# Kernel optimization log

Measured on AMD Instinct MI355X. Metric: run time of the kernel, lower is better.

## Reference

```python
import math
import jax, jax.numpy as jnp
from jax import lax
import numpy as np

LN_EPS = 1e-5
K = 3          # deform-conv kernel size
PAD = 1        # 'same' padding so offset map matches output resolution


def setup_inputs() -> dict:
    key = jax.random.key(0)
    ks = jax.random.split(key, 6)
    B, C, H, W, Co = 4, 256, 64, 64, 256
    x = jax.random.normal(ks[0], (B, C, H, W), jnp.float32)
    dwc_w = jax.random.normal(ks[1], (C, 1, K, K), jnp.float32) * 0.02
    ln_w = jnp.ones((C,), jnp.float32)
    ln_b = jnp.zeros((C,), jnp.float32)
    fcd_w = jax.random.normal(ks[2], (1, C, 1, 1), jnp.float32) * 0.02
    fca_w = jax.random.normal(ks[3], (1, C, 1, 1), jnp.float32) * 0.02
    fan_in = C * K * K
    dconv_w = jax.random.normal(ks[4], (Co, C, K, K), jnp.float32) / math.sqrt(fan_in)
    dconv_b = jnp.zeros((Co,), jnp.float32)
    return dict(x=x, dwc_w=dwc_w, ln_w=ln_w, ln_b=ln_b,
                fcd_w=fcd_w, fca_w=fca_w, dconv_w=dconv_w, dconv_b=dconv_b)


def _bilinear_sample(x, py, px):
    # x: [B,C,H,W]; py/px: [B,KK,H,W] float sample positions (zero-padded border)
    B, C, H, W = x.shape
    y0 = jnp.floor(py); x0 = jnp.floor(px)
    y1 = y0 + 1.0;      x1 = x0 + 1.0
    wy1 = py - y0; wy0 = 1.0 - wy1
    wx1 = px - x0; wx0 = 1.0 - wx1

    def gather(yy, xx):
        valid = ((yy >= 0) & (yy < H) & (xx >= 0) & (xx < W)).astype(x.dtype)
        iy = jnp.clip(yy, 0, H - 1).astype(jnp.int32)
        ix = jnp.clip(xx, 0, W - 1).astype(jnp.int32)
        # per-batch fancy gather -> [B,C,KK,H,W]
        v = jax.vmap(lambda img, a, b: img[:, a, b])(x, iy, ix)
        return v * valid[:, None]

    return (gather(y0, x0) * (wy0 * wx0)[:, None]
          + gather(y0, x1) * (wy0 * wx1)[:, None]
          + gather(y1, x0) * (wy1 * wx0)[:, None]
          + gather(y1, x1) * (wy1 * wx1)[:, None])


def reference(x, dwc_w, ln_w, ln_b, fcd_w, fca_w, dconv_w, dconv_b):
    B, C, H, W = x.shape
    KK = K * K
    # --- offset branch ---
    h = lax.conv_general_dilated(x, dwc_w, (1, 1), ((1, 1), (1, 1)),
                                 dimension_numbers=('NCHW', 'OIHW', 'NCHW'),
                                 feature_group_count=C)
    mu = h.mean(axis=1, keepdims=True)
    var = h.var(axis=1, keepdims=True)
    h = (h - mu) * lax.rsqrt(var + LN_EPS)
    h = h * ln_w[None, :, None, None] + ln_b[None, :, None, None]
    h = jax.nn.relu(h)
    r = jax.nn.relu(jnp.einsum('bchw,oc->bohw', h, fcd_w[:, :, 0, 0]))      # [B,1,H,W]
    t = jnp.einsum('bchw,oc->bohw', h, fca_w[:, :, 0, 0])
    theta = (t / (1.0 + jnp.abs(t))) * (math.pi / 180.0)                     # softsign * pi/180
    ox = r * jnp.cos(theta)
    oy = r * jnp.sin(theta)
    # torch code: offsets = cat([ox tiled KK, oy tiled KK], dim=1) -> [B,2KK,H,W]
    off = jnp.concatenate([jnp.tile(ox, (1, KK, 1, 1)), jnp.tile(oy, (1, KK, 1, 1))], axis=1)
    # torchvision DeformConv2d convention: channel 2k = dy, channel 2k+1 = dx
    dy = off[:, 0::2]   # [B,KK,H,W]
    dx = off[:, 1::2]
    # --- deformable sampling ---
    ky = jnp.repeat(jnp.arange(K), K).astype(x.dtype)   # kernel row per tap
    kx = jnp.tile(jnp.arange(K), K).astype(x.dtype)     # kernel col per tap
    py = (jnp.arange(H, dtype=x.dtype) - PAD)[None, None, :, None] + ky[None, :, None, None] + dy
    px = (jnp.arange(W, dtype=x.dtype) - PAD)[None, None, None, :] + kx[None, :, None, None] + dx
    sampled = _bilinear_sample(x, py, px)               # [B,C,KK,H,W]
    Co = dconv_w.shape[0]
    out = jnp.einsum('bckhw,ock->bohw', sampled, dconv_w.reshape(Co, C, KK))
    return out + dconv_b[None, :, None, None]
```

## Files before the change

kernel.cpp:

```cpp
#include <hip/hip_runtime.h>
#include <hip/hip_bf16.h>

#define B_   4
#define C_   256
#define CO_  256
#define H_   64
#define W_   64
#define HW_  4096

typedef __attribute__((ext_vector_type(8))) short short8;
typedef __attribute__((ext_vector_type(4))) float f32x4;
typedef __attribute__((ext_vector_type(2))) float f32x2;

static __device__ __forceinline__ unsigned short f2bf(float f) {
    unsigned u = __builtin_bit_cast(unsigned, f);
    unsigned r = (u + 0x7fffu + ((u >> 16) & 1u)) >> 16;
    return (unsigned short)r;
}
static __device__ __forceinline__ f32x2 pk_mul(f32x2 a, f32x2 b) {
    f32x2 d; asm("v_pk_mul_f32 %0, %1, %2" : "=v"(d) : "v"(a), "v"(b)); return d;
}
static __device__ __forceinline__ f32x2 pk_fma(f32x2 a, f32x2 b, f32x2 c) {
    f32x2 d; asm("v_pk_fma_f32 %0, %1, %2, %3" : "=v"(d) : "v"(a), "v"(b), "v"(c)); return d;
}
static __device__ __forceinline__ f32x2 pk_add(f32x2 a, f32x2 b) {
    f32x2 d; asm("v_pk_add_f32 %0, %1, %2" : "=v"(d) : "v"(a), "v"(b)); return d;
}
static __device__ __forceinline__ unsigned cvtpk(float a, float b) {
    unsigned r; asm("v_cvt_pk_bf16_f32 %0, %1, %2" : "=v"(r) : "v"(a), "v"(b)); return r;
}
static __device__ __forceinline__ f32x2 unpack_bf2(unsigned d) {
    f32x2 v;
    v.x = __builtin_bit_cast(float, d << 16);
    v.y = __builtin_bit_cast(float, d & 0xffff0000u);
    return v;
}

__global__ void k_transpose(const float* __restrict__ x, unsigned short* __restrict__ xT)
{
    __shared__ float t[32][132];
    int bid = blockIdx.x;
    int b   = bid >> 8;
    int rem = bid & 255;
    int hwT = rem >> 1, cT = rem & 1;
    int hw0 = hwT * 32, c0 = cT * 128;
    int tid = threadIdx.x;
    const float* src = x + (size_t)b * C_ * HW_;
    {
        int hw4 = (tid & 7) << 2;
        int cr  = tid >> 3;
#pragma unroll
        for (int it = 0; it < 4; ++it) {
            int c = cr + it * 32;
            f32x4 v = *(const f32x4*)(src + (size_t)(c0 + c) * HW_ + hw0 + hw4);
            t[hw4 + 0][c] = v.x;
            t[hw4 + 1][c] = v.y;
            t[hw4 + 2][c] = v.z;
            t[hw4 + 3][c] = v.w;
        }
    }
    __syncthreads();
    {
        int c8  = (tid & 15) << 3;
        int hwr = tid >> 4;
        unsigned short* dst = xT + (size_t)(((b << 12) + hw0) * 256) + c0 + c8;
#pragma unroll
        for (int it = 0; it < 2; ++it) {
            int hw = hwr + it * 16;
            f32x4 va = *(const f32x4*)&t[hw][c8];
            f32x4 vb = *(const f32x4*)&t[hw][c8 + 4];
            uint4 u;
            u.x = cvtpk(va.x, va.y);
            u.y = cvtpk(va.z, va.w);
            u.z = cvtpk(vb.x, vb.y);
            u.w = cvtpk(vb.z, vb.w);
            *(uint4*)(dst + (size_t)hw * 256) = u;
        }
    }
}

__global__ void k_packB(const float* __restrict__ w, unsigned short* __restrict__ Bt,
                        const float* __restrict__ dwc_w, float* __restrict__ dwcT)
{
    int bid = blockIdx.x;
    int tid = threadIdx.x;
    if (bid < 9) dwcT[bid * 256 + tid] = dwc_w[tid * 9 + bid];
    int e = bid * 256 + tid;
    int j   = e & 7;
    int l4  = (e >> 3) & 3;
    int l15 = (e >> 5) & 15;
    int ks  = (e >> 9) & 7;
    int og  = (e >> 12) & 15;
    int k   = e >> 16;
    int o = og * 16 + l15;
    int c = ks * 32 + l4 * 8 + j;
    Bt[e] = f2bf(w[(o * C_ + c) * 9 + k]);
}

__launch_bounds__(512, 4)
__global__ void k_main(const unsigned short* __restrict__ xT,
                       const float* __restrict__ dwcT,
                       const float* __restrict__ ln_w,
                       const float* __restrict__ ln_b,
                       const float* __restrict__ fcd_w,
                       const float* __restrict__ fca_w,
                       const unsigned short* __restrict__ Bt,
                       const float* __restrict__ bias,
                       float* __restrict__ out)
{
    __shared__ __align__(16) unsigned char smem[33024];

    int tid = threadIdx.x;
    int bi = blockIdx.x;
    int g = ((bi & 7) << 6) | (bi >> 3);
    int p0 = g << 5;
    int b = p0 >> 12;
    int y = (p0 >> 6) & 63;
    int xh = p0 & 63;

    int lane = tid & 63, wid = tid >> 6;
    int l15 = lane & 15, l4 = lane >> 4;

    int gpos = tid >> 4;
    int csub = tid & 15;
    const unsigned short* xb = xT + (size_t)b * HW_ * C_;
    const char* xbB = (const char*)xb;

    float ox, oy;
    {
        int ch0 = csub << 4;
        f32x2 acc2[8];
#pragma unroll
        for (int i = 0; i < 8; ++i) { acc2[i].x = 0.f; acc2[i].y = 0.f; }
#pragma unroll
        for (int j = 0; j < 9; ++j) {
            int gy = y + j / 3 - 1, gx = xh + gpos + j % 3 - 1;
            if (gy >= 0 && gy < H_ && gx >= 0 && gx < W_) {
                const unsigned short* p = xb + (size_t)((gy << 6) + gx) * 256 + ch0;
                short8 rlo = *(const short8*)(p);
                short8 rhi = *(const short8*)(p + 8);
                const float* wrow = dwcT + j * 256 + ch0;
#pragma unroll
                for (int q = 0; q < 4; ++q) {
                    f32x4 wv = *(const f32x4*)(wrow + q * 4);
                    f32x2 w01v; w01v.x = wv.x; w01v.y = wv.y;
                    f32x2 w23v; w23v.x = wv.z; w23v.y = wv.w;
                    unsigned lo = (q < 2) ? ((unsigned*)&rlo)[q * 2] : ((unsigned*)&rhi)[(q - 2) * 2];
                    unsigned hi = (q < 2) ? ((unsigned*)&rlo)[q * 2 + 1] : ((unsigned*)&rhi)[(q - 2) * 2 + 1];
                    acc2[q * 2 + 0] = pk_fma(unpack_bf2(lo), w01v, acc2[q * 2 + 0]);
                    acc2[q * 2 + 1] = pk_fma(unpack_bf2(hi), w23v, acc2[q * 2 + 1]);
                }
            }
        }
        f32x2 sum2, sq2;
        sum2.x = 0.f; sum2.y = 0.f; sq2.x = 0.f; sq2.y = 0.f;
#pragma unroll
        for (int i = 0; i < 8; ++i) {
            sum2 = pk_add(sum2, acc2[i]);
            sq2  = pk_fma(acc2[i], acc2[i], sq2);
        }
        float s1 = sum2.x + sum2.y, s2 = sq2.x + sq2.y;
#pragma unroll
        for (int m = 1; m <= 8; m <<= 1) {
            s1 += __shfl_xor(s1, m);
            s2 += __shfl_xor(s2, m);
        }
        float mu  = s1 * (1.f / 256.f);
        float var = s2 * (1.f / 256.f) - mu * mu;
        float rs  = rsqrtf(var + 1e-5f);
        float d1 = 0.f, d2 = 0.f;
#pragma unroll
        for (int q = 0; q < 4; ++q) {
            f32x4 lwv = *(const f32x4*)(ln_w  + ch0 + q * 4);
            f32x4 lbv = *(const f32x4*)(ln_b  + ch0 + q * 4);
            f32x4 fdv = *(const f32x4*)(fcd_w + ch0 + q * 4);
            f32x4 fav = *(const f32x4*)(fca_w + ch0 + q * 4);
#pragma unroll
            for (int i = 0; i < 4; ++i) {
                float av = (i & 1) ? acc2[q * 2 + (i >> 1)].y : acc2[q * 2 + (i >> 1)].x;
                float hn = (av - mu) * rs * lwv[i] + lbv[i];
                hn = fmaxf(hn, 0.f);
                d1 = fmaf(hn, fdv[i], d1);
                d2 = fmaf(hn, fav[i], d2);
            }
        }
#pragma unroll
        for (int m = 1; m <= 8; m <<= 1) {
            d1 += __shfl_xor(d1, m);
            d2 += __shfl_xor(d2, m);
        }
        float r0 = fmaxf(d1, 0.f);
        float theta = d2 / (1.f + fabsf(d2)) * 0.017453292519943295f;
        ox = r0 * cosf(theta);
        oy = r0 * sinf(theta);
    }

    f32x4 acc[2][2];
#pragma unroll
    for (int m = 0; m < 2; ++m)
#pragma unroll
        for (int n = 0; n < 2; ++n) {
            acc[m][n].x = 0.f; acc[m][n].y = 0.f; acc[m][n].z = 0.f; acc[m][n].w = 0.f;
        }

    const unsigned short* bwave = Bt + (unsigned)(wid * 2) * 4096u
                                     + (unsigned)(l15 * 32 + l4 * 8);
    unsigned rowb = (unsigned)gpos * 512u;
    unsigned csub16 = (unsigned)csub << 4;
    unsigned swzcol = csub16 ^ (((unsigned)gpos & 7u) << 4);

#define GADDR(k)                                                                  \
        int ky = (k) / 3, kx = (k) - ky * 3;                                      \
        float dyv = ((k) <= 4) ? ox : oy;                                         \
        float dxv = ((k) <= 3) ? ox : oy;                                         \
        float py = (float)(y - 1 + ky) + dyv;                                     \
        float px = (float)(xh + gpos - 1 + kx) + dxv;                             \
        float y0f = floorf(py), x0f = floorf(px);                                 \
        int y0 = (int)y0f, x0 = (int)x0f;                                         \
        int y1 = y0 + 1, x1 = x0 + 1;                                             \
        float wy1 = py - y0f, wy0 = 1.f - wy1;                                    \
        float wx1 = px - x0f, wx0 = 1.f - wx1;                                    \
        float vy0 = (y0 >= 0 && y0 < H_) ? 1.f : 0.f;                             \
        float vy1 = (y1 >= 0 && y1 < H_) ? 1.f : 0.f;                             \
        float vx0 = (x0 >= 0 && x0 < W_) ? 1.f : 0.f;                             \
        float vx1 = (x1 >= 0 && x1 < W_) ? 1.f : 0.f;                             \
        w00 = wy0 * wx0 * vy0 * vx0; w01 = wy0 * wx1 * vy0 * vx1;                 \
        w10 = wy1 * wx0 * vy1 * vx0; w11 = wy1 * wx1 * vy1 * vx1;                 \
        int y0c = min(max(y0, 0), H_ - 1), y1c = min(max(y1, 0), H_ - 1);         \
        int x0c = min(max(x0, 0), W_ - 1), x1c = min(max(x1, 0), W_ - 1);         \
        o00 = (unsigned)((y0c << 6) + x0c) * 512u + csub16;                       \
        o01 = (unsigned)((y0c << 6) + x1c) * 512u + csub16;                       \
        o10 = (unsigned)((y1c << 6) + x0c) * 512u + csub16;                       \
        o11 = (unsigned)((y1c << 6) + x1c) * 512u + csub16;

#define GATHER_TAP(k, buf)                                                        \
    {   unsigned o00, o01, o10, o11;                                              \
        float w00, w01, w10, w11;                                                 \
        GADDR(k);                                                                 \
        f32x2 W00, W01, W10, W11;                                                 \
        W00.x = w00; W00.y = w00; W01.x = w01; W01.y = w01;                       \
        W10.x = w10; W10.y = w10; W11.x = w11; W11.y = w11;                       \
        unsigned wb = (unsigned)(buf) * 16384u + rowb + swzcol;                   \
        _Pragma("unroll")                                                         \
        for (int cq = 0; cq < 2; ++cq) {                                          \
            short8 r00 = *(const short8*)(xbB + o00 + cq * 256);                  \
            short8 r01 = *(const short8*)(xbB + o01 + cq * 256);                  \
            short8 r10 = *(const short8*)(xbB + o10 + cq * 256);                  \
            short8 r11 = *(const short8*)(xbB + o11 + cq * 256);                  \
            uint4 pkv;                                                            \
            _Pragma("unroll")                                                     \
            for (int dw = 0; dw < 4; ++dw) {                                      \
                f32x2 a2 = pk_mul(unpack_bf2(((unsigned*)&r00)[dw]), W00);        \
                a2 = pk_fma(unpack_bf2(((unsigned*)&r01)[dw]), W01, a2);          \
                a2 = pk_fma(unpack_bf2(((unsigned*)&r10)[dw]), W10, a2);          \
                a2 = pk_fma(unpack_bf2(((unsigned*)&r11)[dw]), W11, a2);          \
                ((unsigned*)&pkv)[dw] = cvtpk(a2.x, a2.y);                        \
            }                                                                     \
            *(uint4*)(smem + wb + cq * 256) = pkv;                                \
        }                                                                         \
    }

    GATHER_TAP(0, 0);
    __syncthreads();

#pragma unroll
    for (int k = 0; k < 9; ++k) {
        int t = k & 1;
        {
            const unsigned short* bk = bwave + (unsigned)k * 65536u;
            unsigned abase = (unsigned)t * 16384u;
#pragma unroll
            for (int ks = 0; ks < 8; ++ks) {
                short8 bf0 = *(const short8*)(bk + ks * 512);
                short8 bf1 = *(const short8*)(bk + 4096 + ks * 512);
                unsigned coff = (unsigned)(ks * 64 + (l4 << 4)) ^ (((unsigned)l15 & 7u) << 4);
                short8 a0 = *(const short8*)(smem + abase + (unsigned)l15 * 512u + coff);
                short8 a1 = *(const short8*)(smem + abase + (unsigned)(16 + l15) * 512u + coff);
                acc[0][0] = __builtin_amdgcn_mfma_f32_16x16x32_bf16(a0, bf0, acc[0][0], 0, 0, 0);
                acc[0][1] = __builtin_amdgcn_mfma_f32_16x16x32_bf16(a0, bf1, acc[0][1], 0, 0, 0);
                acc[1][0] = __builtin_amdgcn_mfma_f32_16x16x32_bf16(a1, bf0, acc[1][0], 0, 0, 0);
                acc[1][1] = __builtin_amdgcn_mfma_f32_16x16x32_bf16(a1, bf1, acc[1][1], 0, 0, 0);
            }
        }
        if (k < 8) {
            GATHER_TAP(k + 1, t ^ 1);
        }
        __syncthreads();
    }

    float* epi = (float*)smem;
#pragma unroll
    for (int m = 0; m < 2; ++m)
#pragma unroll
        for (int n = 0; n < 2; ++n)
#pragma unroll
            for (int i = 0; i < 4; ++i) {
                int row = m * 16 + l4 * 4 + i;
                int col = wid * 32 + n * 16 + l15;
                epi[row * 257 + col] = acc[m][n][i];
            }
    __syncthreads();
    int o  = tid >> 1;
    int wq = (tid & 1) << 4;
    float bv = bias[o];
    float* orow = out + (size_t)(((b * CO_ + o) * H_ + y) * W_) + xh + wq;
#pragma unroll
    for (int j = 0; j < 16; j += 4) {
        f32x4 v;
        v.x = epi[(wq + j + 0) * 257 + o] + bv;
        v.y = epi[(wq + j + 1) * 257 + o] + bv;
        v.z = epi[(wq + j + 2) * 257 + o] + bv;
        v.w = epi[(wq + j + 3) * 257 + o] + bv;
        *(f32x4*)(orow + j) = v;
    }
}

extern "C" void kernel_launch(void* const* d_in, const int* in_sizes, int n_in,
                              void* d_out, int out_size, void* d_ws, size_t ws_size,
                              hipStream_t stream) {
    const float* x      = (const float*)d_in[0];
    const float* dwc_w  = (const float*)d_in[1];
    const float* ln_w   = (const float*)d_in[2];
    const float* ln_b   = (const float*)d_in[3];
    const float* fcd_w  = (const float*)d_in[4];
    const float* fca_w  = (const float*)d_in[5];
    const float* dconv_w= (const float*)d_in[6];
    const float* dconv_b= (const float*)d_in[7];
    float* out = (float*)d_out;

    unsigned char* ws = (unsigned char*)d_ws;
    unsigned short* xT = (unsigned short*)(ws);
    unsigned short* Bt = (unsigned short*)(ws + 8388608);
    float* dwcT        = (float*)(ws + 9568256);

    k_transpose<<<1024, 256, 0, stream>>>(x, xT);
    k_packB<<<2304, 256, 0, stream>>>(dconv_w, Bt, dwc_w, dwcT);
    k_main<<<512, 512, 0, stream>>>(xT, dwcT, ln_w, ln_b, fcd_w, fca_w, Bt, dconv_b, out);
}
```

Before: 78.08 us.

## Split offset computation into separate kernel and retile main GEMM to 64x128

Moves the depthwise-conv, layernorm and offset computation into a new k_offsets kernel that writes per-pixel ox/oy to workspace. k_main now tiles a full 64-pixel row against half of the output channels, with each wave computing 4 M-fragments against one B fragment. LDS use doubles to 64KB. The intent is better B-operand reuse and a lighter main kernel. In exchange it adds a kernel launch, an extra pass over the offset maps, and gathers every sampled pixel twice (once per output-channel half).

```diff
diff --git a/kernel.cpp b/kernel.cpp
--- a/kernel.cpp
+++ b/kernel.cpp
@@ -97,19 +97,14 @@
     Bt[e] = f2bf(w[(o * C_ + c) * 9 + k]);
 }
 
-__launch_bounds__(512, 4)
-__global__ void k_main(const unsigned short* __restrict__ xT,
-                       const float* __restrict__ dwcT,
-                       const float* __restrict__ ln_w,
-                       const float* __restrict__ ln_b,
-                       const float* __restrict__ fcd_w,
-                       const float* __restrict__ fca_w,
-                       const unsigned short* __restrict__ Bt,
-                       const float* __restrict__ bias,
-                       float* __restrict__ out)
+__global__ void k_offsets(const unsigned short* __restrict__ xT,
+                          const float* __restrict__ dwcT,
+                          const float* __restrict__ ln_w,
+                          const float* __restrict__ ln_b,
+                          const float* __restrict__ fcd_w,
+                          const float* __restrict__ fca_w,
+                          float* __restrict__ OX, float* __restrict__ OY)
 {
-    __shared__ __align__(16) unsigned char smem[33024];
-
     int tid = threadIdx.x;
     int bi = blockIdx.x;
     int g = ((bi & 7) << 6) | (bi >> 3);
@@ -117,104 +112,121 @@
     int b = p0 >> 12;
     int y = (p0 >> 6) & 63;
     int xh = p0 & 63;
+    int gpos = tid >> 4;
+    int csub = tid & 15;
+    int ch0 = csub << 4;
+    const unsigned short* xb = xT + (size_t)b * HW_ * C_;
+
+    f32x2 acc2[8];
+#pragma unroll
+    for (int i = 0; i < 8; ++i) { acc2[i].x = 0.f; acc2[i].y = 0.f; }
+#pragma unroll
+    for (int j = 0; j < 9; ++j) {
+        int gy = y + j / 3 - 1, gx = xh + gpos + j % 3 - 1;
+        if (gy >= 0 && gy < H_ && gx >= 0 && gx < W_) {
+            const unsigned short* p = xb + (size_t)((gy << 6) + gx) * 256 + ch0;
+            short8 rlo = *(const short8*)(p);
+            short8 rhi = *(const short8*)(p + 8);
+            const float* wrow = dwcT + j * 256 + ch0;
+#pragma unroll
+            for (int q = 0; q < 4; ++q) {
+                f32x4 wv = *(const f32x4*)(wrow + q * 4);
+                f32x2 w01v; w01v.x = wv.x; w01v.y = wv.y;
+                f32x2 w23v; w23v.x = wv.z; w23v.y = wv.w;
+                unsigned lo = (q < 2) ? ((unsigned*)&rlo)[q * 2] : ((unsigned*)&rhi)[(q - 2) * 2];
+                unsigned hi = (q < 2) ? ((unsigned*)&rlo)[q * 2 + 1] : ((unsigned*)&rhi)[(q - 2) * 2 + 1];
+                acc2[q * 2 + 0] = pk_fma(unpack_bf2(lo), w01v, acc2[q * 2 + 0]);
+                acc2[q * 2 + 1] = pk_fma(unpack_bf2(hi), w23v, acc2[q * 2 + 1]);
+            }
+        }
+    }
+    f32x2 sum2, sq2;
+    sum2.x = 0.f; sum2.y = 0.f; sq2.x = 0.f; sq2.y = 0.f;
+#pragma unroll
+    for (int i = 0; i < 8; ++i) {
+        sum2 = pk_add(sum2, acc2[i]);
+        sq2  = pk_fma(acc2[i], acc2[i], sq2);
+    }
+    float s1 = sum2.x + sum2.y, s2 = sq2.x + sq2.y;
+#pragma unroll
+    for (int m = 1; m <= 8; m <<= 1) {
+        s1 += __shfl_xor(s1, m);
+        s2 += __shfl_xor(s2, m);
+    }
+    float mu  = s1 * (1.f / 256.f);
+    float var = s2 * (1.f / 256.f) - mu * mu;
+    float rs  = rsqrtf(var + 1e-5f);
+    float d1 = 0.f, d2 = 0.f;
+#pragma unroll
+    for (int q = 0; q < 4; ++q) {
+        f32x4 lwv = *(const f32x4*)(ln_w  + ch0 + q * 4);
+        f32x4 lbv = *(const f32x4*)(ln_b  + ch0 + q * 4);
+        f32x4 fdv = *(const f32x4*)(fcd_w + ch0 + q * 4);
+        f32x4 fav = *(const f32x4*)(fca_w + ch0 + q * 4);
+#pragma unroll
+        for (int i = 0; i < 4; ++i) {
+            float av = (i & 1) ? acc2[q * 2 + (i >> 1)].y : acc2[q * 2 + (i >> 1)].x;
+            float hn = (av - mu) * rs * lwv[i] + lbv[i];
+            hn = fmaxf(hn, 0.f);
+            d1 = fmaf(hn, fdv[i], d1);
+            d2 = fmaf(hn, fav[i], d2);
+        }
+    }
+#pragma unroll
+    for (int m = 1; m <= 8; m <<= 1) {
+        d1 += __shfl_xor(d1, m);
+        d2 += __shfl_xor(d2, m);
+    }
+    if (csub == 0) {
+        float r0 = fmaxf(d1, 0.f);
+        float theta = d2 / (1.f + fabsf(d2)) * 0.017453292519943295f;
+        int pos = p0 + gpos;
+        OX[pos] = r0 * cosf(theta);
+        OY[pos] = r0 * sinf(theta);
+    }
+}
+
+__launch_bounds__(512, 4)
+__global__ void k_main(const unsigned short* __restrict__ xT,
+                       const float* __restrict__ OX, const float* __restrict__ OY,
+                       const unsigned short* __restrict__ Bt,
+                       const float* __restrict__ bias,
+                       float* __restrict__ out)
+{
+    __shared__ __align__(16) unsigned char smem[65536];
+
+    int tid = threadIdx.x;
+    int bi = blockIdx.x;
+    int g = ((bi & 7) << 6) | (bi >> 3);
+    int tile = g >> 1;
+    int n0g = g & 1;
+    int b = tile >> 6;
+    int y = tile & 63;
 
     int lane = tid & 63, wid = tid >> 6;
     int l15 = lane & 15, l4 = lane >> 4;
 
-    int gpos = tid >> 4;
-    int csub = tid & 15;
-    const unsigned short* xb = xT + (size_t)b * HW_ * C_;
-    const char* xbB = (const char*)xb;
-
-    float ox, oy;
-    {
-        int ch0 = csub << 4;
-        f32x2 acc2[8];
-#pragma unroll
-        for (int i = 0; i < 8; ++i) { acc2[i].x = 0.f; acc2[i].y = 0.f; }
-#pragma unroll
-        for (int j = 0; j < 9; ++j) {
-            int gy = y + j / 3 - 1, gx = xh + gpos + j % 3 - 1;
-            if (gy >= 0 && gy < H_ && gx >= 0 && gx < W_) {
-                const unsigned short* p = xb + (size_t)((gy << 6) + gx) * 256 + ch0;
-                short8 rlo = *(const short8*)(p);
-                short8 rhi = *(const short8*)(p + 8);
-                const float* wrow = dwcT + j * 256 + ch0;
-#pragma unroll
-                for (int q = 0; q < 4; ++q) {
-                    f32x4 wv = *(const f32x4*)(wrow + q * 4);
-                    f32x2 w01v; w01v.x = wv.x; w01v.y = wv.y;
-                    f32x2 w23v; w23v.x = wv.z; w23v.y = wv.w;
-                    unsigned lo = (q < 2) ? ((unsigned*)&rlo)[q * 2] : ((unsigned*)&rhi)[(q - 2) * 2];
-                    unsigned hi = (q < 2) ? ((unsigned*)&rlo)[q * 2 + 1] : ((unsigned*)&rhi)[(q - 2) * 2 + 1];
-                    acc2[q * 2 + 0] = pk_fma(unpack_bf2(lo), w01v, acc2[q * 2 + 0]);
-                    acc2[q * 2 + 1] = pk_fma(unpack_bf2(hi), w23v, acc2[q * 2 + 1]);
-                }
-            }
-        }
-        f32x2 sum2, sq2;
-        sum2.x = 0.f; sum2.y = 0.f; sq2.x = 0.f; sq2.y = 0.f;
-#pragma unroll
-        for (int i = 0; i < 8; ++i) {
-            sum2 = pk_add(sum2, acc2[i]);
-            sq2  = pk_fma(acc2[i], acc2[i], sq2);
-        }
-        float s1 = sum2.x + sum2.y, s2 = sq2.x + sq2.y;
-#pragma unroll
-        for (int m = 1; m <= 8; m <<= 1) {
-            s1 += __shfl_xor(s1, m);
-            s2 += __shfl_xor(s2, m);
-        }
-        float mu  = s1 * (1.f / 256.f);
-        float var = s2 * (1.f / 256.f) - mu * mu;
-        float rs  = rsqrtf(var + 1e-5f);
-        float d1 = 0.f, d2 = 0.f;
-#pragma unroll
-        for (int q = 0; q < 4; ++q) {
-            f32x4 lwv = *(const f32x4*)(ln_w  + ch0 + q * 4);
-            f32x4 lbv = *(const f32x4*)(ln_b  + ch0 + q * 4);
-            f32x4 fdv = *(const f32x4*)(fcd_w + ch0 + q * 4);
-            f32x4 fav = *(const f32x4*)(fca_w + ch0 + q * 4);
-#pragma unroll
-            for (int i = 0; i < 4; ++i) {
-                float av = (i & 1) ? acc2[q * 2 + (i >> 1)].y : acc2[q * 2 + (i >> 1)].x;
-                float hn = (av - mu) * rs * lwv[i] + lbv[i];
-                hn = fmaxf(hn, 0.f);
-                d1 = fmaf(hn, fdv[i], d1);
-                d2 = fmaf(hn, fav[i], d2);
-            }
-        }
-#pragma unroll
-        for (int m = 1; m <= 8; m <<= 1) {
-            d1 += __shfl_xor(d1, m);
-            d2 += __shfl_xor(d2, m);
-        }
-        float r0 = fmaxf(d1, 0.f);
-        float theta = d2 / (1.f + fabsf(d2)) * 0.017453292519943295f;
-        ox = r0 * cosf(theta);
-        oy = r0 * sinf(theta);
-    }
-
-    f32x4 acc[2][2];
-#pragma unroll
-    for (int m = 0; m < 2; ++m)
-#pragma unroll
-        for (int n = 0; n < 2; ++n) {
-            acc[m][n].x = 0.f; acc[m][n].y = 0.f; acc[m][n].z = 0.f; acc[m][n].w = 0.f;
-        }
-
-    const unsigned short* bwave = Bt + (unsigned)(wid * 2) * 4096u
+    f32x4 acc[4];
+#pragma unroll
+    for (int m = 0; m < 4; ++m) {
+        acc[m].x = 0.f; acc[m].y = 0.f; acc[m].z = 0.f; acc[m].w = 0.f;
+    }
+
+    int gpos = tid >> 3;
+    unsigned csub16 = ((unsigned)tid & 7u) << 4;
+    const char* xbB = (const char*)(xT + (size_t)b * HW_ * C_);
+    const unsigned short* bwave = Bt + (unsigned)(n0g * 8 + wid) * 4096u
                                      + (unsigned)(l15 * 32 + l4 * 8);
     unsigned rowb = (unsigned)gpos * 512u;
-    unsigned csub16 = (unsigned)csub << 4;
     unsigned swzcol = csub16 ^ (((unsigned)gpos & 7u) << 4);
+    float ox = OX[(tile << 6) + gpos], oy = OY[(tile << 6) + gpos];
 
 #define GADDR(k)                                                                  \
         int ky = (k) / 3, kx = (k) - ky * 3;                                      \
         float dyv = ((k) <= 4) ? ox : oy;                                         \
         float dxv = ((k) <= 3) ? ox : oy;                                         \
         float py = (float)(y - 1 + ky) + dyv;                                     \
-        float px = (float)(xh + gpos - 1 + kx) + dxv;                             \
+        float px = (float)(gpos - 1 + kx) + dxv;                                  \
         float y0f = floorf(py), x0f = floorf(px);                                 \
         int y0 = (int)y0f, x0 = (int)x0f;                                         \
         int y1 = y0 + 1, x1 = x0 + 1;                                             \
@@ -240,13 +252,13 @@
         f32x2 W00, W01, W10, W11;                                                 \
         W00.x = w00; W00.y = w00; W01.x = w01; W01.y = w01;                       \
         W10.x = w10; W10.y = w10; W11.x = w11; W11.y = w11;                       \
-        unsigned wb = (unsigned)(buf) * 16384u + rowb + swzcol;                   \
+        unsigned wb = (unsigned)(buf) * 32768u + rowb + swzcol;                   \
         _Pragma("unroll")                                                         \
-        for (int cq = 0; cq < 2; ++cq) {                                          \
-            short8 r00 = *(const short8*)(xbB + o00 + cq * 256);                  \
-            short8 r01 = *(const short8*)(xbB + o01 + cq * 256);                  \
-            short8 r10 = *(const short8*)(xbB + o10 + cq * 256);                  \
-            short8 r11 = *(const short8*)(xbB + o11 + cq * 256);                  \
+        for (int cq = 0; cq < 4; ++cq) {                                          \
+            short8 r00 = *(const short8*)(xbB + o00 + cq * 128);                  \
+            short8 r01 = *(const short8*)(xbB + o01 + cq * 128);                  \
+            short8 r10 = *(const short8*)(xbB + o10 + cq * 128);                  \
+            short8 r11 = *(const short8*)(xbB + o11 + cq * 128);                  \
             uint4 pkv;                                                            \
             _Pragma("unroll")                                                     \
             for (int dw = 0; dw < 4; ++dw) {                                      \
@@ -256,7 +268,7 @@
                 a2 = pk_fma(unpack_bf2(((unsigned*)&r11)[dw]), W11, a2);          \
                 ((unsigned*)&pkv)[dw] = cvtpk(a2.x, a2.y);                        \
             }                                                                     \
-            *(uint4*)(smem + wb + cq * 256) = pkv;                                \
+            *(uint4*)(smem + wb + cq * 128) = pkv;                                \
         }                                                                         \
     }
 
@@ -268,18 +280,17 @@
         int t = k & 1;
         {
             const unsigned short* bk = bwave + (unsigned)k * 65536u;
-            unsigned abase = (unsigned)t * 16384u;
+            unsigned abase = (unsigned)t * 32768u;
 #pragma unroll
             for (int ks = 0; ks < 8; ++ks) {
-                short8 bf0 = *(const short8*)(bk + ks * 512);
-                short8 bf1 = *(const short8*)(bk + 4096 + ks * 512);
+                short8 bf = *(const short8*)(bk + ks * 512);
                 unsigned coff = (unsigned)(ks * 64 + (l4 << 4)) ^ (((unsigned)l15 & 7u) << 4);
-                short8 a0 = *(const short8*)(smem + abase + (unsigned)l15 * 512u + coff);
-                short8 a1 = *(const short8*)(smem + abase + (unsigned)(16 + l15) * 512u + coff);
-                acc[0][0] = __builtin_amdgcn_mfma_f32_16x16x32_bf16(a0, bf0, acc[0][0], 0, 0, 0);
-                acc[0][1] = __builtin_amdgcn_mfma_f32_16x16x32_bf16(a0, bf1, acc[0][1], 0, 0, 0);
-                acc[1][0] = __builtin_amdgcn_mfma_f32_16x16x32_bf16(a1, bf0, acc[1][0], 0, 0, 0);
-                acc[1][1] = __builtin_amdgcn_mfma_f32_16x16x32_bf16(a1, bf1, acc[1][1], 0, 0, 0);
+#pragma unroll
+                for (int mf = 0; mf < 4; ++mf) {
+                    short8 a = *(const short8*)(smem + abase +
+                                 (unsigned)(mf * 16 + l15) * 512u + coff);
+                    acc[mf] = __builtin_amdgcn_mfma_f32_16x16x32_bf16(a, bf, acc[mf], 0, 0, 0);
+                }
             }
         }
         if (k < 8) {
@@ -290,27 +301,25 @@
 
     float* epi = (float*)smem;
 #pragma unroll
-    for (int m = 0; m < 2; ++m)
-#pragma unroll
-        for (int n = 0; n < 2; ++n)
-#pragma unroll
-            for (int i = 0; i < 4; ++i) {
-                int row = m * 16 + l4 * 4 + i;
-                int col = wid * 32 + n * 16 + l15;
-                epi[row * 257 + col] = acc[m][n][i];
-            }
+    for (int mf = 0; mf < 4; ++mf)
+#pragma unroll
+        for (int i = 0; i < 4; ++i) {
+            int row = mf * 16 + l4 * 4 + i;
+            int col = wid * 16 + l15;
+            epi[row * 133 + col] = acc[mf][i];
+        }
     __syncthreads();
-    int o  = tid >> 1;
-    int wq = (tid & 1) << 4;
-    float bv = bias[o];
-    float* orow = out + (size_t)(((b * CO_ + o) * H_ + y) * W_) + xh + wq;
+    int o  = tid >> 2;
+    int wq = (tid & 3) << 4;
+    float bv = bias[n0g * 128 + o];
+    float* orow = out + (size_t)(((b * CO_ + n0g * 128 + o) * H_ + y) * W_) + wq;
 #pragma unroll
     for (int j = 0; j < 16; j += 4) {
         f32x4 v;
-        v.x = epi[(wq + j + 0) * 257 + o] + bv;
-        v.y = epi[(wq + j + 1) * 257 + o] + bv;
-        v.z = epi[(wq + j + 2) * 257 + o] + bv;
-        v.w = epi[(wq + j + 3) * 257 + o] + bv;
+        v.x = epi[(wq + j + 0) * 133 + o] + bv;
+        v.y = epi[(wq + j + 1) * 133 + o] + bv;
+        v.z = epi[(wq + j + 2) * 133 + o] + bv;
+        v.w = epi[(wq + j + 3) * 133 + o] + bv;
         *(f32x4*)(orow + j) = v;
     }
 }
@@ -332,8 +341,11 @@
     unsigned short* xT = (unsigned short*)(ws);
     unsigned short* Bt = (unsigned short*)(ws + 8388608);
     float* dwcT        = (float*)(ws + 9568256);
+    float* OX          = (float*)(ws + 9577472);
+    float* OY          = (float*)(ws + 9643008);
 
     k_transpose<<<1024, 256, 0, stream>>>(x, xT);
     k_packB<<<2304, 256, 0, stream>>>(dconv_w, Bt, dwc_w, dwcT);
-    k_main<<<512, 512, 0, stream>>>(xT, dwcT, ln_w, ln_b, fcd_w, fca_w, Bt, dconv_b, out);
-}
+    k_offsets<<<512, 512, 0, stream>>>(xT, dwcT, ln_w, ln_b, fcd_w, fca_w, OX, OY);
+    k_main<<<512, 512, 0, stream>>>(xT, OX, OY, Bt, dconv_b, out);
+}
```

Result: faster. 76.39 us (-2.2%).
